# Performance work log

Measured on AMD Instinct MI355X. Metric: run time of the kernel, lower is better.

The kernel has to match this reference:

```python
import jax, jax.numpy as jnp
import numpy as np
from jax import lax

B, DIM, F, H, W = 2, 256, 4, 16, 16
HEADS, DIM_HEAD, GROUPS = 8, 64, 4
INNER = HEADS * DIM_HEAD            # 512
OFF_DIMS = INNER // GROUPS          # 128
CPB_DIM = DIM // 4                  # 64
DS = (2, 2, 2)                      # downsample_factor
OFFSET_SCALE = (2.0, 2.0, 2.0)


def norm_coords(coords, sizes):
    # coords: (..., 3) in (f, h, w) index units -> normalized to [-1, 1]
    s = jnp.array([max(sizes[0] - 1, 1), max(sizes[1] - 1, 1), max(sizes[2] - 1, 1)], dtype=coords.dtype)
    return 2.0 * coords / s - 1.0


def grid_sample_3d(vol, grid):
    # Faithful to F.grid_sample(..., mode='bilinear', padding_mode='zeros', align_corners=False)
    # vol: (N, C, D, H, W); grid: (N, P, 3) with last dim (x, y, z) -> (W, H, D) axes
    N, C, D, Hh, Ww = vol.shape
    P = grid.shape[1]
    ix = ((grid[..., 0] + 1.0) * Ww - 1.0) * 0.5
    iy = ((grid[..., 1] + 1.0) * Hh - 1.0) * 0.5
    iz = ((grid[..., 2] + 1.0) * D - 1.0) * 0.5
    x0, y0, z0 = jnp.floor(ix), jnp.floor(iy), jnp.floor(iz)
    tx, ty, tz = ix - x0, iy - y0, iz - z0
    vol_flat = vol.reshape(N, C, D * Hh * Ww)
    out = jnp.zeros((N, C, P), vol.dtype)
    for dz in (0, 1):
        for dy in (0, 1):
            for dx in (0, 1):
                xc, yc, zc = x0 + dx, y0 + dy, z0 + dz
                wgt = (jnp.where(dx, tx, 1.0 - tx) * jnp.where(dy, ty, 1.0 - ty) * jnp.where(dz, tz, 1.0 - tz))
                valid = ((xc >= 0) & (xc < Ww) & (yc >= 0) & (yc < Hh) & (zc >= 0) & (zc < D))
                xi = jnp.clip(xc, 0, Ww - 1).astype(jnp.int32)
                yi = jnp.clip(yc, 0, Hh - 1).astype(jnp.int32)
                zi = jnp.clip(zc, 0, D - 1).astype(jnp.int32)
                idx = (zi * Hh + yi) * Ww + xi                      # (N, P)
                vals = jnp.take_along_axis(vol_flat, jnp.broadcast_to(idx[:, None, :], (N, C, P)), axis=2)
                out = out + vals * (wgt * valid)[:, None, :]
    return out


def setup_inputs():
    key = jax.random.key(0)
    ks = jax.random.split(key, 16)
    r = lambda i, shape: jax.random.normal(ks[i], shape, dtype=jnp.float32) * 0.05
    return {
        'x': jax.random.normal(ks[0], (B, DIM, F, H, W), dtype=jnp.float32),
        'wq': r(1, (GROUPS, OFF_DIMS, DIM // GROUPS)),
        'wk': r(2, (GROUPS, OFF_DIMS, DIM // GROUPS)),
        'wv': r(3, (GROUPS, OFF_DIMS, DIM // GROUPS)),
        'off_dw_w': r(4, (OFF_DIMS, 1, 4, 4, 4)),
        'off_dw_b': r(5, (OFF_DIMS,)),
        'off_pw_w': r(6, (3, OFF_DIMS)),
        'cpb_w0': r(7, (3, CPB_DIM)),
        'cpb_b0': r(8, (CPB_DIM,)),
        'cpb_w1': r(9, (CPB_DIM, CPB_DIM)),
        'cpb_b1': r(10, (CPB_DIM,)),
        'cpb_w2': r(11, (CPB_DIM, HEADS // GROUPS)),
        'cpb_b2': r(12, (HEADS // GROUPS,)),
        'wo': r(13, (DIM, INNER)),
        'bo': r(14, (DIM,)),
    }


def reference(x, wq, wk, wv, off_dw_w, off_dw_b, off_pw_w, cpb_w0, cpb_b0, cpb_w1, cpb_b1, cpb_w2, cpb_b2, wo, bo):
    b = x.shape[0]
    f, h, w = x.shape[-3:]
    Pq = f * h * w
    scale = DIM_HEAD ** -0.5

    # grouped 1x1 conv to queries: channels are (g, d_out) ordered
    xg = x.reshape(b, GROUPS, DIM // GROUPS, Pq)
    q = jnp.einsum('bgip,goi->bgop', xg, wq)                        # (b, G, 128, Pq)

    # learned offsets: depthwise strided conv -> GELU -> 1x1 -> tanh -> scale
    gq = q.reshape(b * GROUPS, OFF_DIMS, f, h, w)
    off = lax.conv_general_dilated(gq, off_dw_w, window_strides=DS, padding=[(1, 1)] * 3,
                                   dimension_numbers=('NCDHW', 'OIDHW', 'NCDHW'),
                                   feature_group_count=OFF_DIMS)
    off = jax.nn.gelu(off + off_dw_b[None, :, None, None, None], approximate=False)
    off = jnp.einsum('ncdhw,oc->nodhw', off, off_pw_w)              # (bG, 3, fd, hd, wd)
    off = jnp.tanh(off) * jnp.array(OFFSET_SCALE, off.dtype)[None, :, None, None, None]

    fd, hd, wd = off.shape[-3:]
    Pj = fd * hd * wd
    base = jnp.stack(jnp.meshgrid(jnp.arange(fd), jnp.arange(hd), jnp.arange(wd), indexing='ij'), axis=0).astype(off.dtype)
    vgrid = base[None] + off
    vgrid_scaled = norm_coords(jnp.moveaxis(vgrid, 1, -1), (fd, hd, wd))  # (bG, fd, hd, wd, 3)
    grid_kv = vgrid_scaled.reshape(b * GROUPS, Pj, 3)

    # irregular gather of grouped features at deformed locations
    kv = grid_sample_3d(x.reshape(b * GROUPS, DIM // GROUPS, f, h, w), grid_kv)  # (bG, 64, Pj)
    kvg = kv.reshape(b, GROUPS, DIM // GROUPS, Pj)
    k = jnp.einsum('bgip,goi->bgop', kvg, wk)
    v = jnp.einsum('bgip,goi->bgop', kvg, wv)

    qh = (q * scale).reshape(b, HEADS, DIM_HEAD, Pq)
    kh = k.reshape(b, HEADS, DIM_HEAD, Pj)
    vh = v.reshape(b, HEADS, DIM_HEAD, Pj)
    sim = jnp.einsum('bhdi,bhdj->bhij', qh, kh)                     # (b, H, Pq, Pj)

    # CPB relative-position bias over (log-signed) pairwise grid differences
    baseq = jnp.stack(jnp.meshgrid(jnp.arange(f), jnp.arange(h), jnp.arange(w), indexing='ij'), axis=-1).astype(x.dtype)
    grid_q = norm_coords(baseq, (f, h, w)).reshape(Pq, 3)
    pos = grid_q[None, :, None, :] - grid_kv[:, None, :, :]         # (bG, Pq, Pj, 3)
    bias = jnp.sign(pos) * jnp.log1p(jnp.abs(pos))
    bias = jax.nn.relu(bias @ cpb_w0 + cpb_b0)
    bias = jax.nn.relu(bias @ cpb_w1 + cpb_b1)
    bias = bias @ cpb_w2 + cpb_b2                                   # (bG, Pq, Pj, H//G)
    bias = bias.reshape(b, GROUPS, Pq, Pj, HEADS // GROUPS)
    bias = jnp.transpose(bias, (0, 1, 4, 2, 3)).reshape(b, HEADS, Pq, Pj)

    attn = jax.nn.softmax(sim + bias, axis=-1)
    out = jnp.einsum('bhij,bhdj->bhdi', attn, vh).reshape(b, INNER, Pq)
    out = jnp.einsum('bcp,oc->bop', out, wo) + bo[None, :, None]
    return out.reshape(b, DIM, f, h, w)
```

## Files before the change

kernel.cpp:

```cpp
#include <hip/hip_runtime.h>
#include <hip/hip_bf16.h>
#include <hip/hip_fp16.h>
#include <math.h>

#define BB 2
#define DIMC 256
#define FF 4
#define HH 16
#define WW 16
#define GRP 4
#define CPG 64
#define ODIM 128
#define PQ 1024
#define PJ 128
#define NBG 8
#define INNERC 512

typedef _Float16 f16x8 __attribute__((ext_vector_type(8)));
typedef _Float16 f16x2 __attribute__((ext_vector_type(2)));
typedef float f32x4 __attribute__((ext_vector_type(4)));
typedef float f32x2 __attribute__((ext_vector_type(2)));

__global__ __launch_bounds__(512) void k_qdw(
    const float* __restrict__ x, const float* __restrict__ wq,
    const float* __restrict__ dww, const float* __restrict__ dwb,
    float* __restrict__ q, float* __restrict__ act) {
    __shared__ float qs[1024 * 4];
    int og = blockIdx.x & 31, bg = blockIdx.x >> 5;
    int b = bg >> 2, g = bg & 3;
    int o0 = og * 4;
    int tid = threadIdx.x;
    const float* xp = x + (size_t)(b * DIMC + g * CPG) * PQ;
    const float* wp = wq + (size_t)(g * ODIM + o0) * CPG;

    float accq[2][4] = {};
    #pragma unroll 8
    for (int i = 0; i < CPG; ++i) {
        float wv[4];
        #pragma unroll
        for (int k = 0; k < 4; ++k) wv[k] = wp[k * CPG + i];
        #pragma unroll
        for (int pi = 0; pi < 2; ++pi) {
            float xv = xp[(size_t)i * PQ + tid + pi * 512];
            #pragma unroll
            for (int k = 0; k < 4; ++k) accq[pi][k] += xv * wv[k];
        }
    }
    #pragma unroll
    for (int pi = 0; pi < 2; ++pi) {
        int p = tid + pi * 512;
        *(float4*)&qs[p * 4] = make_float4(accq[pi][0], accq[pi][1], accq[pi][2], accq[pi][3]);
        #pragma unroll
        for (int k = 0; k < 4; ++k)
            q[(size_t)(bg * ODIM + o0 + k) * PQ + p] = accq[pi][k];
    }
    __syncthreads();

    {
        int cl = tid & 3, j = tid >> 2;
        int c = o0 + cl;
        int xo = j & 7, yo = (j >> 3) & 7, zo = j >> 6;
        const float* wd = dww + c * 64;
        float acc = dwb[c];
        #pragma unroll
        for (int kz = 0; kz < 4; ++kz) {
            int z = 2 * zo - 1 + kz;
            if (z < 0 || z >= FF) continue;
            #pragma unroll
            for (int ky = 0; ky < 4; ++ky) {
                int y = 2 * yo - 1 + ky;
                if (y < 0 || y >= HH) continue;
                #pragma unroll
                for (int kx = 0; kx < 4; ++kx) {
                    int xx = 2 * xo - 1 + kx;
                    if (xx < 0 || xx >= WW) continue;
                    acc += qs[((z * HH + y) * WW + xx) * 4 + cl] * wd[(kz * 4 + ky) * 4 + kx];
                }
            }
        }
        act[((size_t)bg * PJ + j) * ODIM + c] =
            0.5f * acc * (1.0f + erff(acc * 0.70710678118654752f));
    }
}

__global__ __launch_bounds__(256) void k_kvf(
    const float* __restrict__ act, const float* __restrict__ pw,
    const float* __restrict__ x, const float* __restrict__ wk,
    const float* __restrict__ wv, float* __restrict__ gkv,
    float* __restrict__ kk2, float* __restrict__ vvT2) {
    __shared__ float red2[2][6];
    __shared__ float crd[2][3];
    __shared__ float kvs[2][64];
    int blk = blockIdx.x;
    int jt = blk & 63, bg = blk >> 6;
    int b = bg >> 2, g = bg & 3;
    int tid = threadIdx.x;
    int half = tid >> 7;
    int t = tid & 127;
    int j = jt * 2 + half;
    int wv_ = t >> 6;

    float val = act[((size_t)bg * PJ + j) * ODIM + t];
    float s0 = val * pw[t];
    float s1 = val * pw[ODIM + t];
    float s2 = val * pw[2 * ODIM + t];
    #pragma unroll
    for (int off = 32; off; off >>= 1) {
        s0 += __shfl_xor(s0, off);
        s1 += __shfl_xor(s1, off);
        s2 += __shfl_xor(s2, off);
    }
    if ((t & 63) == 0) {
        red2[half][wv_ * 3] = s0; red2[half][wv_ * 3 + 1] = s1; red2[half][wv_ * 3 + 2] = s2;
    }
    __syncthreads();
    if (t == 0) {
        s0 = red2[half][0] + red2[half][3];
        s1 = red2[half][1] + red2[half][4];
        s2 = red2[half][2] + red2[half][5];
        float xo = (float)(j & 7), yo = (float)((j >> 3) & 7), zo = (float)(j >> 6);
        float vf = zo + 2.f * tanhf(s0);
        float vh = yo + 2.f * tanhf(s1);
        float vw = xo + 2.f * tanhf(s2);
        float c0 = 2.f * vf - 1.f;
        float c1 = 2.f * vh / 7.f - 1.f;
        float c2 = 2.f * vw / 7.f - 1.f;
        crd[half][0] = c0; crd[half][1] = c1; crd[half][2] = c2;
        gkv[(bg * PJ + j) * 3 + 0] = c0;
        gkv[(bg * PJ + j) * 3 + 1] = c1;
        gkv[(bg * PJ + j) * 3 + 2] = c2;
    }
    __syncthreads();

    if (t < 64) {
        float ix = ((crd[half][0] + 1.f) * WW - 1.f) * 0.5f;
        float iy = ((crd[half][1] + 1.f) * HH - 1.f) * 0.5f;
        float iz = ((crd[half][2] + 1.f) * FF - 1.f) * 0.5f;
        float x0f = floorf(ix), y0f = floorf(iy), z0f = floorf(iz);
        float tx = ix - x0f, ty = iy - y0f, tz = iz - z0f;
        int x0 = (int)x0f, y0 = (int)y0f, z0 = (int)z0f;
        const float* vol = x + (size_t)(b * DIMC + g * CPG + t) * PQ;
        float acc = 0.f;
        #pragma unroll
        for (int dz = 0; dz < 2; ++dz) {
            int zc = z0 + dz;
            if (zc < 0 || zc >= FF) continue;
            float wz = dz ? tz : 1.f - tz;
            #pragma unroll
            for (int dy = 0; dy < 2; ++dy) {
                int yc = y0 + dy;
                if (yc < 0 || yc >= HH) continue;
                float wy = dy ? ty : 1.f - ty;
                #pragma unroll
                for (int dx = 0; dx < 2; ++dx) {
                    int xc = x0 + dx;
                    if (xc < 0 || xc >= WW) continue;
                    float wgt = wz * wy * (dx ? tx : 1.f - tx);
                    acc += vol[(zc * HH + yc) * WW + xc] * wgt;
                }
            }
        }
        kvs[half][t] = acc;
    }
    __syncthreads();

    const float* wkp = wk + (size_t)(g * ODIM + t) * CPG;
    const float* wvp = wv + (size_t)(g * ODIM + t) * CPG;
    float ak = 0.f, av = 0.f;
    #pragma unroll
    for (int i = 0; i < 64; i += 4) {
        float4 kv4 = *(const float4*)&kvs[half][i];
        float4 wk4 = *(const float4*)&wkp[i];
        float4 wv4 = *(const float4*)&wvp[i];
        ak += kv4.x * wk4.x + kv4.y * wk4.y + kv4.z * wk4.z + kv4.w * wk4.w;
        av += kv4.x * wv4.x + kv4.y * wv4.y + kv4.z * wv4.z + kv4.w * wv4.w;
    }
    kk2[((size_t)(bg * 64 + (t & 63)) * PJ + j) * 2 + (t >> 6)] = ak;
    vvT2[((size_t)(bg * 64 + (j >> 1)) * ODIM + t) * 2 + (j & 1)] = av;
}

__global__ __launch_bounds__(256) void k_cpa(
    const float* __restrict__ q, const float* __restrict__ kk2,
    const float* __restrict__ vvT2, const float* __restrict__ gkv,
    const float* __restrict__ w0, const float* __restrict__ b0,
    const float* __restrict__ w1, const float* __restrict__ b1,
    const float* __restrict__ w2, const float* __restrict__ b2,
    float* __restrict__ outh) {
    __shared__ __align__(16) float tbuf[4 * 2176];
    __shared__ __align__(16) float biasL[16 * 256];
    __shared__ float redA[64];
    float* attL = tbuf;
    float* qsL  = tbuf + 4096;

    int blk = blockIdx.x;
    int it = blk & 63, bg = blk >> 6;
    int b = bg >> 2, g = bg & 3;
    int tid = threadIdx.x;
    int w = tid >> 6, lane = tid & 63, col = lane & 15, quad = lane >> 4;

    uint4 bfr[2][4];
    #pragma unroll
    for (int kc = 0; kc < 2; ++kc)
        #pragma unroll
        for (int nt = 0; nt < 4; ++nt) {
            int n = nt * 16 + col;
            int kbase = kc * 32 + quad * 8;
            unsigned int pk[4];
            #pragma unroll
            for (int p = 0; p < 4; ++p) {
                f16x2 hv = {(_Float16)w1[(kbase + 2 * p) * 64 + n],
                            (_Float16)w1[(kbase + 2 * p + 1) * 64 + n]};
                pk[p] = *(unsigned int*)&hv;
            }
            bfr[kc][nt] = make_uint4(pk[0], pk[1], pk[2], pk[3]);
        }

    f16x2 w0a[2][4], w0b[2][4], w0c[2][4], b0h[2][4];
    #pragma unroll
    for (int kc = 0; kc < 2; ++kc) {
        int d0 = kc * 32 + quad * 8;
        #pragma unroll
        for (int pr = 0; pr < 4; ++pr) {
            w0a[kc][pr] = (f16x2){(_Float16)w0[d0 + 2 * pr], (_Float16)w0[d0 + 2 * pr + 1]};
            w0b[kc][pr] = (f16x2){(_Float16)w0[64 + d0 + 2 * pr], (_Float16)w0[64 + d0 + 2 * pr + 1]};
            w0c[kc][pr] = (f16x2){(_Float16)w0[128 + d0 + 2 * pr], (_Float16)w0[128 + d0 + 2 * pr + 1]};
            b0h[kc][pr] = (f16x2){(_Float16)b0[d0 + 2 * pr], (_Float16)b0[d0 + 2 * pr + 1]};
        }
    }
    f16x2 zero2 = {(_Float16)0.f, (_Float16)0.f};

    float g0r[8], g1r[8], g2r[8];
    #pragma unroll
    for (int mtg = 0; mtg < 8; ++mtg) {
        int jr = mtg * 16 + col;
        g0r[mtg] = gkv[(bg * PJ + jr) * 3 + 0];
        g1r[mtg] = gkv[(bg * PJ + jr) * 3 + 1];
        g2r[mtg] = gkv[(bg * PJ + jr) * 3 + 2];
    }
    float b1v[4]; f32x2 w2v[4];
    #pragma unroll
    for (int nt = 0; nt < 4; ++nt) {
        int jj = nt * 16 + col;
        b1v[nt] = b1[jj];
        w2v[nt] = *(const f32x2*)&w2[jj * 2];
    }
    f32x2 bias_b2 = *(const f32x2*)b2;
    f32x2* mytb = (f32x2*)&tbuf[w * 2176];

    #pragma unroll 1
    for (int ii = 0; ii < 4; ++ii) {
        int il = w * 4 + ii;
        int i = it * 16 + il;
        int wq_ = i & 15, hq = (i >> 4) & 15, fq = i >> 8;
        float cq0 = 2.f * fq / 3.f - 1.f;
        float cq1 = 2.f * hq / 15.f - 1.f;
        float cq2 = 2.f * wq_ / 15.f - 1.f;

        #pragma unroll 1
        for (int mh = 0; mh < 2; ++mh) {
            f16x2 t0h[4], t1h[4], t2h[4];
            #pragma unroll
            for (int mt = 0; mt < 4; ++mt) {
                int mtg = mh * 4 + mt;
                float p0 = cq0 - g0r[mtg];
                float p1 = cq1 - g1r[mtg];
                float p2 = cq2 - g2r[mtg];
                float t0 = copysignf(__logf(1.f + fabsf(p0)), p0);
                float t1 = copysignf(__logf(1.f + fabsf(p1)), p1);
                float t2 = copysignf(__logf(1.f + fabsf(p2)), p2);
                _Float16 h0 = (_Float16)t0, h1 = (_Float16)t1, h2 = (_Float16)t2;
                t0h[mt] = (f16x2){h0, h0};
                t1h[mt] = (f16x2){h1, h1};
                t2h[mt] = (f16x2){h2, h2};
            }
            f32x4 acc[4][4] = {};
            #pragma unroll
            for (int kc = 0; kc < 2; ++kc) {
                #pragma unroll
                for (int mt = 0; mt < 4; ++mt) {
                    unsigned int pk[4];
                    #pragma unroll
                    for (int pr = 0; pr < 4; ++pr) {
                        f16x2 z = b0h[kc][pr];
                        z += t0h[mt] * w0a[kc][pr];
                        z += t1h[mt] * w0b[kc][pr];
                        z += t2h[mt] * w0c[kc][pr];
                        z = __builtin_elementwise_max(z, zero2);
                        pk[pr] = *(unsigned int*)&z;
                    }
                    uint4 afu = make_uint4(pk[0], pk[1], pk[2], pk[3]);
                    f16x8 af = *(f16x8*)&afu;
                    #pragma unroll
                    for (int nt = 0; nt < 4; ++nt)
                        acc[mt][nt] = __builtin_amdgcn_mfma_f32_16x16x32_f16(
                            af, *(f16x8*)&bfr[kc][nt], acc[mt][nt], 0, 0, 0);
                }
            }
            #pragma unroll
            for (int mt = 0; mt < 4; ++mt)
                #pragma unroll
                for (int reg = 0; reg < 4; ++reg) {
                    f32x2 pp = {0.f, 0.f};
                    #pragma unroll
                    for (int nt = 0; nt < 4; ++nt) {
                        float hv = fmaxf(acc[mt][nt][reg] + b1v[nt], 0.f);
                        pp += hv * w2v[nt];
                    }
                    mytb[(mt * 16 + quad * 4 + reg) * 17 + col] = pp;
                }
            f32x2 s = bias_b2;
            {
                const f32x2* pr2 = mytb + lane * 17;
                #pragma unroll
                for (int c = 0; c < 16; ++c) s += pr2[c];
            }
            int jl = mh * 64 + lane;
            *(f32x2*)&biasL[(il * 128 + jl) * 2] = s;
        }
    }
    __syncthreads();

    int half = tid >> 7;
    int j = tid & 127;

    {
        const float* qp = q + (size_t)(bg * ODIM + j) * PQ + it * 16 + half * 8;
        float4 qa = *(const float4*)qp;
        float4 qb = *(const float4*)(qp + 4);
        int e = j >> 6, d = j & 63;
        qsL[(half * 8 + 0) * 128 + d * 2 + e] = qa.x * 0.125f;
        qsL[(half * 8 + 1) * 128 + d * 2 + e] = qa.y * 0.125f;
        qsL[(half * 8 + 2) * 128 + d * 2 + e] = qa.z * 0.125f;
        qsL[(half * 8 + 3) * 128 + d * 2 + e] = qa.w * 0.125f;
        qsL[(half * 8 + 4) * 128 + d * 2 + e] = qb.x * 0.125f;
        qsL[(half * 8 + 5) * 128 + d * 2 + e] = qb.y * 0.125f;
        qsL[(half * 8 + 6) * 128 + d * 2 + e] = qb.z * 0.125f;
        qsL[(half * 8 + 7) * 128 + d * 2 + e] = qb.w * 0.125f;
    }
    __syncthreads();

    f32x2 sc[8];
    #pragma unroll
    for (int k = 0; k < 8; ++k)
        sc[k] = *(const f32x2*)&biasL[((half * 8 + k) * 128 + j) * 2];

    {
        const f32x2* kp = (const f32x2*)kk2 + (size_t)(bg * 64) * PJ + j;
        const f32x2* qs2 = (const f32x2*)qsL;
        #pragma unroll 4
        for (int d = 0; d < 64; ++d) {
            f32x2 kv2 = kp[(size_t)d * PJ];
            #pragma unroll
            for (int k = 0; k < 8; ++k)
                sc[k] += qs2[(half * 8 + k) * 64 + d] * kv2;
        }
    }
    #pragma unroll
    for (int k = 0; k < 8; ++k) {
        int il = half * 8 + k;
        attL[il * 256 + j] = sc[k].x;
        attL[il * 256 + 128 + j] = sc[k].y;
    }
    __syncthreads();

    #pragma unroll
    for (int rr = 0; rr < 8; ++rr) {
        int r = w * 8 + rr;
        int il = r >> 1, hd = r & 1;
        float a0 = attL[il * 256 + hd * 128 + lane];
        float a1 = attL[il * 256 + hd * 128 + 64 + lane];
        float mx = fmaxf(a0, a1);
        #pragma unroll
        for (int off = 32; off; off >>= 1) mx = fmaxf(mx, __shfl_xor(mx, off));
        float ex = __expf(a0 - mx) + __expf(a1 - mx);
        #pragma unroll
        for (int off = 32; off; off >>= 1) ex += __shfl_xor(ex, off);
        if (lane == 0) { redA[r * 2] = mx; redA[r * 2 + 1] = ex; }
    }
    __syncthreads();
    #pragma unroll
    for (int k = 0; k < 8; ++k) {
        int il = half * 8 + k;
        float p0n = __expf(sc[k].x - redA[(il * 2 + 0) * 2]) * (1.f / redA[(il * 2 + 0) * 2 + 1]);
        float p1n = __expf(sc[k].y - redA[(il * 2 + 1) * 2]) * (1.f / redA[(il * 2 + 1) * 2 + 1]);
        attL[il * 256 + j] = p0n;
        attL[il * 256 + 128 + j] = p1n;
    }
    __syncthreads();

    {
        const f32x2* vp = (const f32x2*)vvT2 + (size_t)(bg * 64) * ODIM + j;
        int e = j >> 6;
        f32x2 oacc[8] = {};
        #pragma unroll 4
        for (int jp = 0; jp < 64; ++jp) {
            f32x2 vv2 = vp[(size_t)jp * ODIM];
            #pragma unroll
            for (int k = 0; k < 8; ++k) {
                f32x2 ap2 = *(const f32x2*)&attL[(half * 8 + k) * 256 + e * 128 + jp * 2];
                oacc[k] += ap2 * vv2;
            }
        }
        #pragma unroll
        for (int k = 0; k < 8; ++k)
            outh[((size_t)b * PQ + it * 16 + half * 8 + k) * INNERC + g * 128 + j] =
                oacc[k].x + oacc[k].y;
    }
}

__global__ __launch_bounds__(256) void k_out(
    const float* __restrict__ outh, const float* __restrict__ wo,
    const float* __restrict__ bo, float* __restrict__ out) {
    __shared__ float At[32][68];
    __shared__ float Bt[32][36];
    int blk = blockIdx.x;
    int nt = blk & 7, mt = blk >> 3;
    int m0 = mt * 64, o0 = nt * 32;
    int tid = threadIdx.x;
    int tm = tid >> 4, tn = tid & 15;
    int mloc = tm * 4, nloc = tn * 2;

    int ra = tid >> 2, ca = (tid & 3) * 8;
    int rb = tid >> 3, cb = (tid & 7) * 4;

    float4 pa0, pa1, pb;
    {
        const float* Ap = outh + (size_t)(m0 + ra) * INNERC + ca;
        pa0 = *(const float4*)Ap;
        pa1 = *(const float4*)(Ap + 4);
        pb = *(const float4*)(wo + (size_t)(o0 + rb) * INNERC + cb);
    }

    float acc[4][2] = {};
    for (int ch = 0; ch < 16; ++ch) {
        #pragma unroll
        for (int k = 0; k < 4; ++k) {
            At[ca + k][ra] = ((const float*)&pa0)[k];
            At[ca + 4 + k][ra] = ((const float*)&pa1)[k];
            Bt[cb + k][rb] = ((const float*)&pb)[k];
        }
        __syncthreads();
        if (ch < 15) {
            int c0 = (ch + 1) * 32;
            const float* Ap = outh + (size_t)(m0 + ra) * INNERC + c0 + ca;
            pa0 = *(const float4*)Ap;
            pa1 = *(const float4*)(Ap + 4);
            pb = *(const float4*)(wo + (size_t)(o0 + rb) * INNERC + c0 + cb);
        }
        #pragma unroll
        for (int kk = 0; kk < 32; ++kk) {
            float4 a4 = *(const float4*)&At[kk][mloc];
            float2 b2 = *(const float2*)&Bt[kk][nloc];
            #pragma unroll
            for (int i = 0; i < 4; ++i) {
                float av = ((const float*)&a4)[i];
                acc[i][0] += av * b2.x;
                acc[i][1] += av * b2.y;
            }
        }
        __syncthreads();
    }

    #pragma unroll
    for (int jn = 0; jn < 2; ++jn) {
        int o = o0 + nloc + jn;
        float bv = bo[o];
        #pragma unroll
        for (int i = 0; i < 4; ++i) {
            int m = m0 + mloc + i;
            int b = m >> 10, p = m & 1023;
            out[((size_t)(b * DIMC + o)) * PQ + p] = acc[i][jn] + bv;
        }
    }
}

extern "C" void kernel_launch(void* const* d_in, const int* in_sizes, int n_in,
                              void* d_out, int out_size, void* d_ws, size_t ws_size,
                              hipStream_t stream) {
    const float* x   = (const float*)d_in[0];
    const float* wq  = (const float*)d_in[1];
    const float* wk  = (const float*)d_in[2];
    const float* wv  = (const float*)d_in[3];
    const float* dww = (const float*)d_in[4];
    const float* dwb = (const float*)d_in[5];
    const float* pw  = (const float*)d_in[6];
    const float* w0  = (const float*)d_in[7];
    const float* b0  = (const float*)d_in[8];
    const float* w1  = (const float*)d_in[9];
    const float* b1  = (const float*)d_in[10];
    const float* w2  = (const float*)d_in[11];
    const float* b2  = (const float*)d_in[12];
    const float* wo  = (const float*)d_in[13];
    const float* bo  = (const float*)d_in[14];
    float* out = (float*)d_out;

    float* ws_f  = (float*)d_ws;
    float* q     = ws_f;
    float* act   = q + 1048576;
    float* gkv   = act + 131072;
    float* kk2   = gkv + 3072;
    float* vvT2  = kk2 + 131072;
    float* outh  = vvT2 + 131072;

    k_qdw<<<256, 512, 0, stream>>>(x, wq, dww, dwb, q, act);
    k_kvf<<<512, 256, 0, stream>>>(act, pw, x, wk, wv, gkv, kk2, vvT2);
    k_cpa<<<512, 256, 0, stream>>>(q, kk2, vvT2, gkv, w0, b0, w1, b1, w2, b2, outh);
    k_out<<<256, 256, 0, stream>>>(outh, wo, bo, out);
}
```

Baseline: 165.4 us.

## Use split-fp16 MFMA for attention QK and PV in fused attention kernel

```diff
diff --git a/kernel.cpp b/kernel.cpp
--- a/kernel.cpp
+++ b/kernel.cpp
@@ -87,7 +87,7 @@
     const float* __restrict__ act, const float* __restrict__ pw,
     const float* __restrict__ x, const float* __restrict__ wk,
     const float* __restrict__ wv, float* __restrict__ gkv,
-    float* __restrict__ kk2, float* __restrict__ vvT2) {
+    _Float16* __restrict__ khT, _Float16* __restrict__ vhT) {
     __shared__ float red2[2][6];
     __shared__ float crd[2][3];
     __shared__ float kvs[2][64];
@@ -175,22 +175,27 @@
         ak += kv4.x * wk4.x + kv4.y * wk4.y + kv4.z * wk4.z + kv4.w * wk4.w;
         av += kv4.x * wv4.x + kv4.y * wv4.y + kv4.z * wv4.z + kv4.w * wv4.w;
     }
-    kk2[((size_t)(bg * 64 + (t & 63)) * PJ + j) * 2 + (t >> 6)] = ak;
-    vvT2[((size_t)(bg * 64 + (j >> 1)) * ODIM + t) * 2 + (j & 1)] = av;
+    {
+        _Float16 khi = (_Float16)ak;
+        khT[((size_t)(bg * 128 + j) * 2 + 0) * 128 + t] = khi;
+        khT[((size_t)(bg * 128 + j) * 2 + 1) * 128 + t] = (_Float16)(ak - (float)khi);
+        _Float16 vhi = (_Float16)av;
+        vhT[((size_t)(bg * 128 + t) * 2 + 0) * 128 + j] = vhi;
+        vhT[((size_t)(bg * 128 + t) * 2 + 1) * 128 + j] = (_Float16)(av - (float)vhi);
+    }
 }
 
 __global__ __launch_bounds__(256) void k_cpa(
-    const float* __restrict__ q, const float* __restrict__ kk2,
-    const float* __restrict__ vvT2, const float* __restrict__ gkv,
+    const float* __restrict__ q, const _Float16* __restrict__ khT,
+    const _Float16* __restrict__ vhT, const float* __restrict__ gkv,
     const float* __restrict__ w0, const float* __restrict__ b0,
     const float* __restrict__ w1, const float* __restrict__ b1,
     const float* __restrict__ w2, const float* __restrict__ b2,
     float* __restrict__ outh) {
     __shared__ __align__(16) float tbuf[4 * 2176];
-    __shared__ __align__(16) float biasL[16 * 256];
-    __shared__ float redA[64];
-    float* attL = tbuf;
-    float* qsL  = tbuf + 4096;
+    __shared__ __align__(16) float biasL[2 * 16 * 132];
+    __shared__ float smax[64];
+    __shared__ float ssum[64];
 
     int blk = blockIdx.x;
     int it = blk & 63, bg = blk >> 6;
@@ -315,96 +320,141 @@
                 for (int c = 0; c < 16; ++c) s += pr2[c];
             }
             int jl = mh * 64 + lane;
-            *(f32x2*)&biasL[(il * 128 + jl) * 2] = s;
-        }
-    }
-    __syncthreads();
-
-    int half = tid >> 7;
-    int j = tid & 127;
+            biasL[il * 132 + jl] = s.x;
+            biasL[(16 + il) * 132 + jl] = s.y;
+        }
+    }
+    __syncthreads();
+
+    _Float16* attFh = (_Float16*)tbuf;
+    _Float16* attFl = attFh + 4352;
+    _Float16* qsFh  = attFh + 8704;
+    _Float16* qsFl  = attFh + 10880;
 
     {
-        const float* qp = q + (size_t)(bg * ODIM + j) * PQ + it * 16 + half * 8;
+        int o = tid & 127, hf = tid >> 7;
+        const float* qp = q + (size_t)(bg * ODIM + o) * PQ + it * 16 + hf * 8;
         float4 qa = *(const float4*)qp;
         float4 qb = *(const float4*)(qp + 4);
-        int e = j >> 6, d = j & 63;
-        qsL[(half * 8 + 0) * 128 + d * 2 + e] = qa.x * 0.125f;
-        qsL[(half * 8 + 1) * 128 + d * 2 + e] = qa.y * 0.125f;
-        qsL[(half * 8 + 2) * 128 + d * 2 + e] = qa.z * 0.125f;
-        qsL[(half * 8 + 3) * 128 + d * 2 + e] = qa.w * 0.125f;
-        qsL[(half * 8 + 4) * 128 + d * 2 + e] = qb.x * 0.125f;
-        qsL[(half * 8 + 5) * 128 + d * 2 + e] = qb.y * 0.125f;
-        qsL[(half * 8 + 6) * 128 + d * 2 + e] = qb.z * 0.125f;
-        qsL[(half * 8 + 7) * 128 + d * 2 + e] = qb.w * 0.125f;
-    }
-    __syncthreads();
-
-    f32x2 sc[8];
-    #pragma unroll
-    for (int k = 0; k < 8; ++k)
-        sc[k] = *(const f32x2*)&biasL[((half * 8 + k) * 128 + j) * 2];
-
-    {
-        const f32x2* kp = (const f32x2*)kk2 + (size_t)(bg * 64) * PJ + j;
-        const f32x2* qs2 = (const f32x2*)qsL;
-        #pragma unroll 4
-        for (int d = 0; d < 64; ++d) {
-            f32x2 kv2 = kp[(size_t)d * PJ];
-            #pragma unroll
-            for (int k = 0; k < 8; ++k)
-                sc[k] += qs2[(half * 8 + k) * 64 + d] * kv2;
-        }
-    }
-    #pragma unroll
-    for (int k = 0; k < 8; ++k) {
-        int il = half * 8 + k;
-        attL[il * 256 + j] = sc[k].x;
-        attL[il * 256 + 128 + j] = sc[k].y;
-    }
-    __syncthreads();
-
-    #pragma unroll
-    for (int rr = 0; rr < 8; ++rr) {
-        int r = w * 8 + rr;
-        int il = r >> 1, hd = r & 1;
-        float a0 = attL[il * 256 + hd * 128 + lane];
-        float a1 = attL[il * 256 + hd * 128 + 64 + lane];
-        float mx = fmaxf(a0, a1);
-        #pragma unroll
-        for (int off = 32; off; off >>= 1) mx = fmaxf(mx, __shfl_xor(mx, off));
-        float ex = __expf(a0 - mx) + __expf(a1 - mx);
-        #pragma unroll
-        for (int off = 32; off; off >>= 1) ex += __shfl_xor(ex, off);
-        if (lane == 0) { redA[r * 2] = mx; redA[r * 2 + 1] = ex; }
-    }
-    __syncthreads();
-    #pragma unroll
-    for (int k = 0; k < 8; ++k) {
-        int il = half * 8 + k;
-        float p0n = __expf(sc[k].x - redA[(il * 2 + 0) * 2]) * (1.f / redA[(il * 2 + 0) * 2 + 1]);
-        float p1n = __expf(sc[k].y - redA[(il * 2 + 1) * 2]) * (1.f / redA[(il * 2 + 1) * 2 + 1]);
-        attL[il * 256 + j] = p0n;
-        attL[il * 256 + 128 + j] = p1n;
-    }
-    __syncthreads();
-
-    {
-        const f32x2* vp = (const f32x2*)vvT2 + (size_t)(bg * 64) * ODIM + j;
-        int e = j >> 6;
-        f32x2 oacc[8] = {};
-        #pragma unroll 4
-        for (int jp = 0; jp < 64; ++jp) {
-            f32x2 vv2 = vp[(size_t)jp * ODIM];
-            #pragma unroll
-            for (int k = 0; k < 8; ++k) {
-                f32x2 ap2 = *(const f32x2*)&attL[(half * 8 + k) * 256 + e * 128 + jp * 2];
-                oacc[k] += ap2 * vv2;
-            }
-        }
-        #pragma unroll
-        for (int k = 0; k < 8; ++k)
-            outh[((size_t)b * PQ + it * 16 + half * 8 + k) * INNERC + g * 128 + j] =
-                oacc[k].x + oacc[k].y;
+        float vals[8] = {qa.x, qa.y, qa.z, qa.w, qb.x, qb.y, qb.z, qb.w};
+        #pragma unroll
+        for (int k = 0; k < 8; ++k) {
+            float v = vals[k] * 0.125f;
+            _Float16 vhi = (_Float16)v;
+            qsFh[(hf * 8 + k) * 136 + o] = vhi;
+            qsFl[(hf * 8 + k) * 136 + o] = (_Float16)(v - (float)vhi);
+        }
+    }
+    __syncthreads();
+
+    int h = w >> 1, jh = w & 1;
+
+    f16x8 aqh[2], aql[2];
+    #pragma unroll
+    for (int kc = 0; kc < 2; ++kc) {
+        aqh[kc] = *(f16x8*)&qsFh[col * 136 + h * 64 + kc * 32 + quad * 8];
+        aql[kc] = *(f16x8*)&qsFl[col * 136 + h * 64 + kc * 32 + quad * 8];
+    }
+    f32x4 acc[4];
+    #pragma unroll
+    for (int jt = 0; jt < 4; ++jt) {
+        int j0 = jh * 64 + jt * 16;
+        #pragma unroll
+        for (int r = 0; r < 4; ++r)
+            acc[jt][r] = biasL[(h * 16 + quad * 4 + r) * 132 + j0 + col];
+    }
+    const _Float16* kbase = khT + (size_t)(bg * 128) * 256 + h * 64 + quad * 8;
+    #pragma unroll
+    for (int kc = 0; kc < 2; ++kc) {
+        #pragma unroll
+        for (int jt = 0; jt < 4; ++jt) {
+            const _Float16* kp = kbase + (size_t)(jh * 64 + jt * 16 + col) * 256 + kc * 32;
+            f16x8 bh = *(const f16x8*)kp;
+            f16x8 bl = *(const f16x8*)(kp + 128);
+            acc[jt] = __builtin_amdgcn_mfma_f32_16x16x32_f16(aqh[kc], bh, acc[jt], 0, 0, 0);
+            acc[jt] = __builtin_amdgcn_mfma_f32_16x16x32_f16(aql[kc], bh, acc[jt], 0, 0, 0);
+            acc[jt] = __builtin_amdgcn_mfma_f32_16x16x32_f16(aqh[kc], bl, acc[jt], 0, 0, 0);
+        }
+    }
+
+    float mrow[4];
+    #pragma unroll
+    for (int r = 0; r < 4; ++r) {
+        float m = fmaxf(fmaxf(acc[0][r], acc[1][r]), fmaxf(acc[2][r], acc[3][r]));
+        #pragma unroll
+        for (int off = 1; off <= 8; off <<= 1) m = fmaxf(m, __shfl_xor(m, off));
+        mrow[r] = m;
+    }
+    if (col == 0) {
+        #pragma unroll
+        for (int r = 0; r < 4; ++r) smax[(h * 2 + jh) * 16 + quad * 4 + r] = mrow[r];
+    }
+    __syncthreads();
+    #pragma unroll
+    for (int r = 0; r < 4; ++r)
+        mrow[r] = fmaxf(smax[(h * 2) * 16 + quad * 4 + r],
+                        smax[(h * 2 + 1) * 16 + quad * 4 + r]);
+
+    float lrow[4] = {0.f, 0.f, 0.f, 0.f};
+    #pragma unroll
+    for (int jt = 0; jt < 4; ++jt) {
+        int j0 = jh * 64 + jt * 16;
+        #pragma unroll
+        for (int r = 0; r < 4; ++r) {
+            float p = __expf(acc[jt][r] - mrow[r]);
+            lrow[r] += p;
+            _Float16 phi = (_Float16)p;
+            attFh[(h * 16 + quad * 4 + r) * 136 + j0 + col] = phi;
+            attFl[(h * 16 + quad * 4 + r) * 136 + j0 + col] = (_Float16)(p - (float)phi);
+        }
+    }
+    #pragma unroll
+    for (int r = 0; r < 4; ++r) {
+        float l = lrow[r];
+        #pragma unroll
+        for (int off = 1; off <= 8; off <<= 1) l += __shfl_xor(l, off);
+        lrow[r] = l;
+    }
+    if (col == 0) {
+        #pragma unroll
+        for (int r = 0; r < 4; ++r) ssum[(h * 2 + jh) * 16 + quad * 4 + r] = lrow[r];
+    }
+    __syncthreads();
+
+    f16x8 pah[4], pal[4];
+    #pragma unroll
+    for (int kc = 0; kc < 4; ++kc) {
+        pah[kc] = *(f16x8*)&attFh[(h * 16 + col) * 136 + kc * 32 + quad * 8];
+        pal[kc] = *(f16x8*)&attFl[(h * 16 + col) * 136 + kc * 32 + quad * 8];
+    }
+    float rinv[4];
+    #pragma unroll
+    for (int r = 0; r < 4; ++r)
+        rinv[r] = 1.f / (ssum[(h * 2) * 16 + quad * 4 + r] +
+                         ssum[(h * 2 + 1) * 16 + quad * 4 + r]);
+
+    f32x4 oacc[2] = {};
+    int chl0 = jh * 32 + col;
+    #pragma unroll
+    for (int kc = 0; kc < 4; ++kc) {
+        #pragma unroll
+        for (int nt = 0; nt < 2; ++nt) {
+            int chl = chl0 + nt * 16;
+            const _Float16* vp = vhT + (size_t)(bg * 128 + h * 64 + chl) * 256 + kc * 32 + quad * 8;
+            f16x8 vh8 = *(const f16x8*)vp;
+            f16x8 vl8 = *(const f16x8*)(vp + 128);
+            oacc[nt] = __builtin_amdgcn_mfma_f32_16x16x32_f16(pah[kc], vh8, oacc[nt], 0, 0, 0);
+            oacc[nt] = __builtin_amdgcn_mfma_f32_16x16x32_f16(pal[kc], vh8, oacc[nt], 0, 0, 0);
+            oacc[nt] = __builtin_amdgcn_mfma_f32_16x16x32_f16(pah[kc], vl8, oacc[nt], 0, 0, 0);
+        }
+    }
+    #pragma unroll
+    for (int nt = 0; nt < 2; ++nt) {
+        int chl = chl0 + nt * 16;
+        #pragma unroll
+        for (int r = 0; r < 4; ++r)
+            outh[((size_t)(b * PQ + it * 16 + quad * 4 + r)) * INNERC + g * 128 + h * 64 + chl] =
+                oacc[nt][r] * rinv[r];
     }
 }
 
@@ -498,12 +548,12 @@
     float* q     = ws_f;
     float* act   = q + 1048576;
     float* gkv   = act + 131072;
-    float* kk2   = gkv + 3072;
-    float* vvT2  = kk2 + 131072;
-    float* outh  = vvT2 + 131072;
+    _Float16* khT = (_Float16*)(gkv + 3072);
+    _Float16* vhT = (_Float16*)(gkv + 3072 + 131072);
+    float* outh  = gkv + 3072 + 262144;
 
     k_qdw<<<256, 512, 0, stream>>>(x, wq, dww, dwb, q, act);
-    k_kvf<<<512, 256, 0, stream>>>(act, pw, x, wk, wv, gkv, kk2, vvT2);
-    k_cpa<<<512, 256, 0, stream>>>(q, kk2, vvT2, gkv, w0, b0, w1, b1, w2, b2, outh);
+    k_kvf<<<512, 256, 0, stream>>>(act, pw, x, wk, wv, gkv, khT, vhT);
+    k_cpa<<<512, 256, 0, stream>>>(q, khT, vhT, gkv, w0, b0, w1, b1, w2, b2, outh);
     k_out<<<256, 256, 0, stream>>>(outh, wo, bo, out);
 }
```

New measurement: 158.0 us. -4.5%, faster.
